# Performance work log

Measured on AMD Instinct MI355X. Metric: run time of the kernel, lower is better.

The kernel has to match this reference:

```python
import jax, jax.numpy as jnp
import numpy as np
import math

T, B, N, D = 4, 4, 1024, 512
H = 8
HD = D // H
EPS = 1e-6


def setup_inputs() -> dict:
    key = jax.random.key(0)
    ks = jax.random.split(key, 9)
    s = 1.0 / math.sqrt(D)
    inp = {"x": jax.random.normal(ks[0], (T, B, N, D), dtype=jnp.float32)}
    names = ["wq", "wk", "wv", "wo"]
    for i, nm in enumerate(names):
        inp[nm] = jax.random.uniform(ks[1 + i], (D, D), dtype=jnp.float32, minval=-s, maxval=s)
        inp["b" + nm[1]] = jax.random.uniform(ks[5 + i], (D,), dtype=jnp.float32, minval=-s, maxval=s)
    return inp


def reference(x, wq, bq, wk, bk, wv, bv, wo, bo):
    t, b, n, d = x.shape
    # torch Linear: y = x @ W.T + bias
    q = x @ wq.T + bq
    k = x @ wk.T + bk
    v = x @ wv.T + bv
    # (t, b, n, H, HD) -> (t, b, H, n, HD)
    qh = q.reshape(t, b, n, H, HD).transpose(0, 1, 3, 2, 4)
    kh = k.reshape(t, b, n, H, HD).transpose(0, 1, 3, 2, 4)
    vh = v.reshape(t, b, n, H, HD).transpose(0, 1, 3, 2, 4)
    scores = jnp.einsum("tbhqd,tbhkd->tbhqk", qh, kh) / math.sqrt(HD)
    attn = jax.nn.relu(scores)
    attn = attn / (attn.sum(axis=-1, keepdims=True) + EPS)
    ctx = jnp.einsum("tbhqk,tbhkd->tbhqd", attn, vh)
    out = ctx.transpose(0, 1, 3, 2, 4).reshape(t, b, n, d)
    return out @ wo.T + bo
```

## Files before the change

### kernel.cpp

```cpp
#include <hip/hip_runtime.h>

typedef unsigned short u16;
typedef __attribute__((ext_vector_type(8))) short bf16x8;
typedef __attribute__((ext_vector_type(4))) float f32x4;

__device__ inline u16 f2b(float f) {
    unsigned u;
    __builtin_memcpy(&u, &f, 4);
    unsigned r = u + 0x7FFF + ((u >> 16) & 1);
    return (u16)(r >> 16);
}

__device__ inline bf16x8 pack8(const float* p) {
    union { u16 us[8]; bf16x8 v; } r;
#pragma unroll
    for (int i = 0; i < 8; i++) r.us[i] = f2b(p[i]);
    return r.v;
}

__device__ inline void gload16(const void* g, void* l) {
    __builtin_amdgcn_global_load_lds((__attribute__((address_space(1))) void*)g,
                                     (__attribute__((address_space(3))) void*)l, 16, 0, 0);
}

__global__ __launch_bounds__(256) void conv_kernel(const float* __restrict__ x,
                                                   const float* __restrict__ wq,
                                                   const float* __restrict__ wk,
                                                   const float* __restrict__ wv,
                                                   const float* __restrict__ wo,
                                                   u16* __restrict__ xb, u16* __restrict__ wb) {
    const int bid = blockIdx.x;
    const float* src;
    u16* dst;
    size_t base;
    if (bid < 4096) {
        src = x; dst = xb; base = (size_t)bid * 2048;
    } else {
        const int wsel = (bid - 4096) >> 7;
        src = (wsel == 0) ? wq : (wsel == 1) ? wk : (wsel == 2) ? wv : wo;
        dst = wb + (size_t)wsel * 262144;
        base = (size_t)((bid - 4096) & 127) * 2048;
    }
    const size_t idx = base + (size_t)threadIdx.x * 8;
    float a[8];
    *(float4*)&a[0] = *(const float4*)&src[idx];
    *(float4*)&a[4] = *(const float4*)&src[idx + 4];
    *(bf16x8*)&dst[idx] = pack8(a);
}

template <int MODE>
__global__ __launch_bounds__(256) void gemm_kernel(const u16* __restrict__ A,
                                                   const u16* __restrict__ W,
                                                   const float* __restrict__ B0,
                                                   const float* __restrict__ B1,
                                                   const float* __restrict__ B2,
                                                   void* __restrict__ O0v, u16* __restrict__ O1,
                                                   u16* __restrict__ O2) {
    const int m0 = blockIdx.x * 128;
    const int n0 = blockIdx.y * 128;
    const int seg = (MODE == 0) ? (n0 >> 9) : 0;
    const int nl0 = (MODE == 0) ? (n0 & 511) : n0;
    const float* Bb = (seg == 0) ? B0 : (seg == 1) ? B1 : B2;
    u16* O = (seg == 0) ? (u16*)O0v : (seg == 1) ? O1 : O2;

    __shared__ __align__(16) u16 Al[128 * 32];
    __shared__ __align__(16) u16 Bl[128 * 32];

    const int tid = threadIdx.x;
    const int lane = tid & 63, wave = tid >> 6;
    const int quad = lane >> 4, col = lane & 15;
    const int wm = wave >> 1, wn = wave & 1;

    f32x4 acc[4][4];
#pragma unroll
    for (int i = 0; i < 4; i++)
#pragma unroll
        for (int j = 0; j < 4; j++) acc[i][j] = (f32x4){0.f, 0.f, 0.f, 0.f};

    for (int k0 = 0; k0 < 512; k0 += 32) {
#pragma unroll
        for (int sh = 0; sh < 4; sh++) {
            const int c = tid + sh * 256;
            const int cl = c & 511;
            const int row = cl >> 2, cc = (cl & 3) * 8;
            if (c < 512)
                gload16(&A[(size_t)(m0 + row) * 512 + k0 + cc], &Al[cl * 8]);
            else
                gload16(&W[(size_t)(n0 + row) * 512 + k0 + cc], &Bl[cl * 8]);
        }
        __syncthreads();
        bf16x8 af[4], bfr[4];
#pragma unroll
        for (int t = 0; t < 4; t++) {
            af[t] = *(const bf16x8*)&Al[(wm * 64 + t * 16 + col) * 32 + quad * 8];
            bfr[t] = *(const bf16x8*)&Bl[(wn * 64 + t * 16 + col) * 32 + quad * 8];
        }
#pragma unroll
        for (int i = 0; i < 4; i++)
#pragma unroll
            for (int j = 0; j < 4; j++)
                acc[i][j] = __builtin_amdgcn_mfma_f32_16x16x32_bf16(af[i], bfr[j], acc[i][j], 0, 0, 0);
        __syncthreads();
    }

    float bias[4];
#pragma unroll
    for (int j = 0; j < 4; j++) bias[j] = Bb[nl0 + wn * 64 + j * 16 + col];

#pragma unroll
    for (int i = 0; i < 4; i++) {
        const int mbase = m0 + wm * 64 + i * 16 + quad * 4;
#pragma unroll
        for (int j = 0; j < 4; j++) {
            const int nl = nl0 + wn * 64 + j * 16 + col;
            if (MODE == 1) {
                float* Of = (float*)O0v;
#pragma unroll
                for (int r = 0; r < 4; r++)
                    Of[(size_t)(mbase + r) * 512 + nl] = acc[i][j][r] + bias[j];
            } else {
                const int h = nl >> 6, hd = nl & 63;
                if (seg < 2) {
                    const float qs = (seg == 0) ? 0.125f : 1.f;
#pragma unroll
                    for (int r = 0; r < 4; r++) {
                        int m = mbase + r;
                        int s = m >> 10, tok = m & 1023;
                        O[(size_t)((s * 8 + h) * 1024 + tok) * 64 + hd] =
                            f2b((acc[i][j][r] + bias[j]) * qs);
                    }
                } else {
                    int s = mbase >> 10, tok0 = mbase & 1023;
                    union { u16 us[4]; uint2 v; } pk;
#pragma unroll
                    for (int r = 0; r < 4; r++) pk.us[r] = f2b(acc[i][j][r] + bias[j]);
                    *(uint2*)&O[(size_t)((s * 8 + h) * 64 + hd) * 1024 + tok0] = pk.v;
                }
            }
        }
    }
}

__global__ __launch_bounds__(256) void attn_kernel(const u16* __restrict__ Q,
                                                   const u16* __restrict__ Kp,
                                                   const u16* __restrict__ Vt,
                                                   u16* __restrict__ Ctx) {
    constexpr int SP = 72;
    __shared__ __align__(16) u16 Kl[4096];
    __shared__ __align__(16) u16 Vl[4096];
    __shared__ __align__(16) u16 pl[4][32 * SP];

    const int bid = blockIdx.x;
    const int head = bid & 127;
    const int qt = bid >> 7;
    const int s = head >> 3, h = head & 7;
    const u16* Qh = Q + (size_t)head * 65536;
    const u16* Kh = Kp + (size_t)head * 65536;
    const u16* Vh = Vt + (size_t)head * 65536;

    const int tid = threadIdx.x;
    const int lane = tid & 63, wave = tid >> 6;
    const int quad = lane >> 4, col = lane & 15;
    const int q0 = qt * 128 + wave * 32;

    int srow[2], sxc[2];
#pragma unroll
    for (int i = 0; i < 2; i++) {
        const int p = tid + i * 256;
        srow[i] = p >> 3;
        sxc[i] = (p & 7) ^ (srow[i] & 7);
    }

    union { u16 us[8]; bf16x8 v; } one;
#pragma unroll
    for (int i = 0; i < 8; i++) one.us[i] = 0x3F80;
    const bf16x8 onesf = one.v;

    bf16x8 qf[2][2];
#pragma unroll
    for (int nt = 0; nt < 2; nt++)
#pragma unroll
        for (int kk = 0; kk < 2; kk++)
            qf[nt][kk] = *(const bf16x8*)&Qh[(size_t)(q0 + nt * 16 + col) * 64 + kk * 32 + quad * 8];

    f32x4 cacc[2][4];
#pragma unroll
    for (int i = 0; i < 2; i++)
#pragma unroll
        for (int j = 0; j < 4; j++) cacc[i][j] = (f32x4){0.f, 0.f, 0.f, 0.f};
    f32x4 dacc[2];
#pragma unroll
    for (int i = 0; i < 2; i++) dacc[i] = (f32x4){0.f, 0.f, 0.f, 0.f};

    const int cxor = col & 7;

    for (int kt = 0; kt < 16; kt++) {
        const int k0 = kt * 64;

#pragma unroll
        for (int i = 0; i < 2; i++) {
            const int p = tid + i * 256;
            gload16(&Kh[(size_t)(k0 + srow[i]) * 64 + sxc[i] * 8], &Kl[p * 8]);
        }
#pragma unroll
        for (int i = 0; i < 2; i++) {
            const int p = tid + i * 256;
            gload16(&Vh[(size_t)srow[i] * 1024 + k0 + sxc[i] * 8], &Vl[p * 8]);
        }
        __syncthreads();

        f32x4 sacc[4][2];
#pragma unroll
        for (int i = 0; i < 4; i++)
#pragma unroll
            for (int j = 0; j < 2; j++) sacc[i][j] = (f32x4){0.f, 0.f, 0.f, 0.f};
#pragma unroll
        for (int kk = 0; kk < 2; kk++) {
            bf16x8 kf[4];
#pragma unroll
            for (int mt = 0; mt < 4; mt++)
                kf[mt] = *(const bf16x8*)&Kl[((mt * 16 + col) * 8 + ((kk * 4 + quad) ^ cxor)) * 8];
#pragma unroll
            for (int mt = 0; mt < 4; mt++)
#pragma unroll
                for (int nt = 0; nt < 2; nt++)
                    sacc[mt][nt] =
                        __builtin_amdgcn_mfma_f32_16x16x32_bf16(kf[mt], qf[nt][kk], sacc[mt][nt], 0, 0, 0);
        }

#pragma unroll
        for (int nt = 0; nt < 2; nt++) {
#pragma unroll
            for (int mt = 0; mt < 4; mt++) {
                unsigned u0 = __float_as_uint(fmaxf(sacc[mt][nt][0], 0.f)) + 0x8000u;
                unsigned u1 = __float_as_uint(fmaxf(sacc[mt][nt][1], 0.f)) + 0x8000u;
                unsigned u2 = __float_as_uint(fmaxf(sacc[mt][nt][2], 0.f)) + 0x8000u;
                unsigned u3 = __float_as_uint(fmaxf(sacc[mt][nt][3], 0.f)) + 0x8000u;
                uint2 pk;
                pk.x = __builtin_amdgcn_perm(u1, u0, 0x07060302);
                pk.y = __builtin_amdgcn_perm(u3, u2, 0x07060302);
                *(uint2*)&pl[wave][(nt * 16 + col) * SP + mt * 16 + quad * 4] = pk;
            }
        }

#pragma unroll
        for (int kk = 0; kk < 2; kk++) {
            bf16x8 pf[2], vf[4];
#pragma unroll
            for (int pt = 0; pt < 2; pt++)
                pf[pt] = *(const bf16x8*)&pl[wave][(pt * 16 + col) * SP + kk * 32 + quad * 8];
#pragma unroll
            for (int nt = 0; nt < 4; nt++)
                vf[nt] = *(const bf16x8*)&Vl[((nt * 16 + col) * 8 + ((kk * 4 + quad) ^ cxor)) * 8];
#pragma unroll
            for (int pt = 0; pt < 2; pt++)
                dacc[pt] = __builtin_amdgcn_mfma_f32_16x16x32_bf16(pf[pt], onesf, dacc[pt], 0, 0, 0);
#pragma unroll
            for (int pt = 0; pt < 2; pt++)
#pragma unroll
                for (int nt = 0; nt < 4; nt++)
                    cacc[pt][nt] =
                        __builtin_amdgcn_mfma_f32_16x16x32_bf16(pf[pt], vf[nt], cacc[pt][nt], 0, 0, 0);
        }
        __syncthreads();
    }

#pragma unroll
    for (int pt = 0; pt < 2; pt++) {
        float inv[4];
#pragma unroll
        for (int r = 0; r < 4; r++) inv[r] = 1.f / (dacc[pt][r] + 1e-6f);
#pragma unroll
        for (int nt = 0; nt < 4; nt++) {
#pragma unroll
            for (int r = 0; r < 4; r++) {
                const int row = pt * 16 + quad * 4 + r;
                const size_t grow = (size_t)(s * 1024 + q0 + row);
                Ctx[grow * 512 + h * 64 + nt * 16 + col] = f2b(cacc[pt][nt][r] * inv[r]);
            }
        }
    }
}

extern "C" void kernel_launch(void* const* d_in, const int* in_sizes, int n_in, void* d_out,
                              int out_size, void* d_ws, size_t ws_size, hipStream_t stream) {
    const float* x = (const float*)d_in[0];
    const float* wq = (const float*)d_in[1];
    const float* bq = (const float*)d_in[2];
    const float* wk = (const float*)d_in[3];
    const float* bk = (const float*)d_in[4];
    const float* wv = (const float*)d_in[5];
    const float* bv = (const float*)d_in[6];
    const float* wo = (const float*)d_in[7];
    const float* bo = (const float*)d_in[8];

    const size_t E = 16384ull * 512ull;
    u16* xb = (u16*)d_ws;
    u16* cw = xb;
    u16* wb = xb + E;
    u16* qw = wb + 4 * 262144;
    u16* kw = qw + E;
    u16* vw = kw + E;

    conv_kernel<<<dim3(4096 + 512), 256, 0, stream>>>(x, wq, wk, wv, wo, xb, wb);
    gemm_kernel<0><<<dim3(128, 12), 256, 0, stream>>>(xb, wb, bq, bk, bv, qw, kw, vw);
    attn_kernel<<<dim3(1024), 256, 0, stream>>>(qw, kw, vw, cw);
    gemm_kernel<1><<<dim3(128, 4), 256, 0, stream>>>(cw, wb + 3 * 262144, bo, nullptr, nullptr,
                                                     d_out, nullptr, nullptr);
}
```

Baseline: 206.3 us.

## Widen GEMM K-tile with swizzled LDS and double attention queries per wave

The GEMM kernel now stages 64-wide K slices per iteration into LDS using an XOR swizzle. This halves the number of barrier pairs and aims to reduce LDS bank conflicts on the fragment reads. The attention kernel now handles 64 queries per wave (256 per block) and launches half as many blocks, so each K/V tile loaded into LDS is reused across twice as many queries. In exchange, register and LDS use per block go up, and the smaller grid may lower occupancy.

```diff
diff --git a/kernel.cpp b/kernel.cpp
--- a/kernel.cpp
+++ b/kernel.cpp
@@ -63,13 +63,22 @@
     const float* Bb = (seg == 0) ? B0 : (seg == 1) ? B1 : B2;
     u16* O = (seg == 0) ? (u16*)O0v : (seg == 1) ? O1 : O2;
 
-    __shared__ __align__(16) u16 Al[128 * 32];
-    __shared__ __align__(16) u16 Bl[128 * 32];
+    __shared__ __align__(16) u16 Al[128 * 64];
+    __shared__ __align__(16) u16 Bl[128 * 64];
 
     const int tid = threadIdx.x;
     const int lane = tid & 63, wave = tid >> 6;
     const int quad = lane >> 4, col = lane & 15;
     const int wm = wave >> 1, wn = wave & 1;
+    const int cxor = col & 7;
+
+    int srow[4], sl[4];
+#pragma unroll
+    for (int i = 0; i < 4; i++) {
+        const int cl = tid + i * 256;
+        srow[i] = cl >> 3;
+        sl[i] = (cl & 7) ^ (srow[i] & 7);
+    }
 
     f32x4 acc[4][4];
 #pragma unroll
@@ -77,29 +86,35 @@
 #pragma unroll
         for (int j = 0; j < 4; j++) acc[i][j] = (f32x4){0.f, 0.f, 0.f, 0.f};
 
-    for (int k0 = 0; k0 < 512; k0 += 32) {
-#pragma unroll
-        for (int sh = 0; sh < 4; sh++) {
-            const int c = tid + sh * 256;
-            const int cl = c & 511;
-            const int row = cl >> 2, cc = (cl & 3) * 8;
-            if (c < 512)
-                gload16(&A[(size_t)(m0 + row) * 512 + k0 + cc], &Al[cl * 8]);
-            else
-                gload16(&W[(size_t)(n0 + row) * 512 + k0 + cc], &Bl[cl * 8]);
+    for (int k0 = 0; k0 < 512; k0 += 64) {
+#pragma unroll
+        for (int i = 0; i < 4; i++) {
+            const int p = tid + i * 256;
+            gload16(&A[(size_t)(m0 + srow[i]) * 512 + k0 + sl[i] * 8], &Al[p * 8]);
+        }
+#pragma unroll
+        for (int i = 0; i < 4; i++) {
+            const int p = tid + i * 256;
+            gload16(&W[(size_t)(n0 + srow[i]) * 512 + k0 + sl[i] * 8], &Bl[p * 8]);
         }
         __syncthreads();
-        bf16x8 af[4], bfr[4];
-#pragma unroll
-        for (int t = 0; t < 4; t++) {
-            af[t] = *(const bf16x8*)&Al[(wm * 64 + t * 16 + col) * 32 + quad * 8];
-            bfr[t] = *(const bf16x8*)&Bl[(wn * 64 + t * 16 + col) * 32 + quad * 8];
-        }
-#pragma unroll
-        for (int i = 0; i < 4; i++)
-#pragma unroll
-            for (int j = 0; j < 4; j++)
-                acc[i][j] = __builtin_amdgcn_mfma_f32_16x16x32_bf16(af[i], bfr[j], acc[i][j], 0, 0, 0);
+#pragma unroll
+        for (int kk = 0; kk < 2; kk++) {
+            bf16x8 af[4], bfr[4];
+#pragma unroll
+            for (int t = 0; t < 4; t++) {
+                const int ra = wm * 64 + t * 16 + col;
+                const int rb = wn * 64 + t * 16 + col;
+                const int slot = (kk * 4 + quad) ^ cxor;
+                af[t] = *(const bf16x8*)&Al[ra * 64 + slot * 8];
+                bfr[t] = *(const bf16x8*)&Bl[rb * 64 + slot * 8];
+            }
+#pragma unroll
+            for (int i = 0; i < 4; i++)
+#pragma unroll
+                for (int j = 0; j < 4; j++)
+                    acc[i][j] = __builtin_amdgcn_mfma_f32_16x16x32_bf16(af[i], bfr[j], acc[i][j], 0, 0, 0);
+        }
         __syncthreads();
     }
 
@@ -148,7 +163,7 @@
     constexpr int SP = 72;
     __shared__ __align__(16) u16 Kl[4096];
     __shared__ __align__(16) u16 Vl[4096];
-    __shared__ __align__(16) u16 pl[4][32 * SP];
+    __shared__ __align__(16) u16 pl[4][64 * SP];
 
     const int bid = blockIdx.x;
     const int head = bid & 127;
@@ -161,14 +176,15 @@
     const int tid = threadIdx.x;
     const int lane = tid & 63, wave = tid >> 6;
     const int quad = lane >> 4, col = lane & 15;
-    const int q0 = qt * 128 + wave * 32;
-
-    int srow[2], sxc[2];
+    const int q0 = qt * 256 + wave * 64;
+    const int cxor = col & 7;
+
+    int srow[2], sl[2];
 #pragma unroll
     for (int i = 0; i < 2; i++) {
         const int p = tid + i * 256;
         srow[i] = p >> 3;
-        sxc[i] = (p & 7) ^ (srow[i] & 7);
+        sl[i] = (p & 7) ^ (srow[i] & 7);
     }
 
     union { u16 us[8]; bf16x8 v; } one;
@@ -176,23 +192,21 @@
     for (int i = 0; i < 8; i++) one.us[i] = 0x3F80;
     const bf16x8 onesf = one.v;
 
-    bf16x8 qf[2][2];
-#pragma unroll
-    for (int nt = 0; nt < 2; nt++)
+    bf16x8 qf[4][2];
+#pragma unroll
+    for (int nt = 0; nt < 4; nt++)
 #pragma unroll
         for (int kk = 0; kk < 2; kk++)
             qf[nt][kk] = *(const bf16x8*)&Qh[(size_t)(q0 + nt * 16 + col) * 64 + kk * 32 + quad * 8];
 
-    f32x4 cacc[2][4];
-#pragma unroll
-    for (int i = 0; i < 2; i++)
+    f32x4 cacc[4][4];
+#pragma unroll
+    for (int i = 0; i < 4; i++)
 #pragma unroll
         for (int j = 0; j < 4; j++) cacc[i][j] = (f32x4){0.f, 0.f, 0.f, 0.f};
-    f32x4 dacc[2];
-#pragma unroll
-    for (int i = 0; i < 2; i++) dacc[i] = (f32x4){0.f, 0.f, 0.f, 0.f};
-
-    const int cxor = col & 7;
+    f32x4 dacc[4];
+#pragma unroll
+    for (int i = 0; i < 4; i++) dacc[i] = (f32x4){0.f, 0.f, 0.f, 0.f};
 
     for (int kt = 0; kt < 16; kt++) {
         const int k0 = kt * 64;
@@ -200,36 +214,36 @@
 #pragma unroll
         for (int i = 0; i < 2; i++) {
             const int p = tid + i * 256;
-            gload16(&Kh[(size_t)(k0 + srow[i]) * 64 + sxc[i] * 8], &Kl[p * 8]);
+            gload16(&Kh[(size_t)(k0 + srow[i]) * 64 + sl[i] * 8], &Kl[p * 8]);
         }
 #pragma unroll
         for (int i = 0; i < 2; i++) {
             const int p = tid + i * 256;
-            gload16(&Vh[(size_t)srow[i] * 1024 + k0 + sxc[i] * 8], &Vl[p * 8]);
+            gload16(&Vh[(size_t)srow[i] * 1024 + k0 + sl[i] * 8], &Vl[p * 8]);
         }
         __syncthreads();
 
-        f32x4 sacc[4][2];
+        f32x4 sacc[4][4];
 #pragma unroll
         for (int i = 0; i < 4; i++)
 #pragma unroll
-            for (int j = 0; j < 2; j++) sacc[i][j] = (f32x4){0.f, 0.f, 0.f, 0.f};
+            for (int j = 0; j < 4; j++) sacc[i][j] = (f32x4){0.f, 0.f, 0.f, 0.f};
 #pragma unroll
         for (int kk = 0; kk < 2; kk++) {
             bf16x8 kf[4];
 #pragma unroll
             for (int mt = 0; mt < 4; mt++)
-                kf[mt] = *(const bf16x8*)&Kl[((mt * 16 + col) * 8 + ((kk * 4 + quad) ^ cxor)) * 8];
+                kf[mt] = *(const bf16x8*)&Kl[(mt * 16 + col) * 64 + (((kk * 4 + quad) ^ cxor)) * 8];
 #pragma unroll
             for (int mt = 0; mt < 4; mt++)
 #pragma unroll
-                for (int nt = 0; nt < 2; nt++)
+                for (int nt = 0; nt < 4; nt++)
                     sacc[mt][nt] =
                         __builtin_amdgcn_mfma_f32_16x16x32_bf16(kf[mt], qf[nt][kk], sacc[mt][nt], 0, 0, 0);
         }
 
 #pragma unroll
-        for (int nt = 0; nt < 2; nt++) {
+        for (int nt = 0; nt < 4; nt++) {
 #pragma unroll
             for (int mt = 0; mt < 4; mt++) {
                 unsigned u0 = __float_as_uint(fmaxf(sacc[mt][nt][0], 0.f)) + 0x8000u;
@@ -245,18 +259,18 @@
 
 #pragma unroll
         for (int kk = 0; kk < 2; kk++) {
-            bf16x8 pf[2], vf[4];
-#pragma unroll
-            for (int pt = 0; pt < 2; pt++)
+            bf16x8 pf[4], vf[4];
+#pragma unroll
+            for (int pt = 0; pt < 4; pt++)
                 pf[pt] = *(const bf16x8*)&pl[wave][(pt * 16 + col) * SP + kk * 32 + quad * 8];
 #pragma unroll
             for (int nt = 0; nt < 4; nt++)
-                vf[nt] = *(const bf16x8*)&Vl[((nt * 16 + col) * 8 + ((kk * 4 + quad) ^ cxor)) * 8];
-#pragma unroll
-            for (int pt = 0; pt < 2; pt++)
+                vf[nt] = *(const bf16x8*)&Vl[(nt * 16 + col) * 64 + (((kk * 4 + quad) ^ cxor)) * 8];
+#pragma unroll
+            for (int pt = 0; pt < 4; pt++)
                 dacc[pt] = __builtin_amdgcn_mfma_f32_16x16x32_bf16(pf[pt], onesf, dacc[pt], 0, 0, 0);
 #pragma unroll
-            for (int pt = 0; pt < 2; pt++)
+            for (int pt = 0; pt < 4; pt++)
 #pragma unroll
                 for (int nt = 0; nt < 4; nt++)
                     cacc[pt][nt] =
@@ -266,7 +280,7 @@
     }
 
 #pragma unroll
-    for (int pt = 0; pt < 2; pt++) {
+    for (int pt = 0; pt < 4; pt++) {
         float inv[4];
 #pragma unroll
         for (int r = 0; r < 4; r++) inv[r] = 1.f / (dacc[pt][r] + 1e-6f);
@@ -304,7 +318,7 @@
 
     conv_kernel<<<dim3(4096 + 512), 256, 0, stream>>>(x, wq, wk, wv, wo, xb, wb);
     gemm_kernel<0><<<dim3(128, 12), 256, 0, stream>>>(xb, wb, bq, bk, bv, qw, kw, vw);
-    attn_kernel<<<dim3(1024), 256, 0, stream>>>(qw, kw, vw, cw);
+    attn_kernel<<<dim3(512), 256, 0, stream>>>(qw, kw, vw, cw);
     gemm_kernel<1><<<dim3(128, 4), 256, 0, stream>>>(cw, wb + 3 * 262144, bo, nullptr, nullptr,
                                                      d_out, nullptr, nullptr);
 }
```

Measured after the change: 228.3 us. 1.11x slower.
